# Kernel tuning notes

Hardware: AMD Instinct MI355X
Metric: run time of the kernel (lower is better)

The kernel has to match this reference:

```python
import jax, jax.numpy as jnp
import numpy as np

N, C, R = 100000, 128, 3
NUM_EMB = 3  # ceil((r+1)/2)+1 for r=3
E0, EL = 300000, 80000
SC = 0.05


def setup_inputs() -> dict:
    key = jax.random.key(0)
    ks = jax.random.split(key, 40)
    d = {}
    d["x"] = jax.random.normal(ks[0], (N, C), jnp.float32)
    # loopyN0: row 0 = sorted target node ids (CSR requirement), row 1 = neighbor ids
    t0 = jnp.sort(jax.random.randint(ks[1], (E0,), 0, N))
    s0 = jax.random.randint(ks[2], (E0,), 0, N)
    d["loopyN0"] = jnp.stack([t0, s0]).astype(jnp.int32)
    for L in range(1, R + 1):
        tgt = jnp.sort(jax.random.randint(ks[2 + 2 * L], (EL,), 0, N))
        rest = jax.random.randint(ks[3 + 2 * L], (L + 1, EL), 0, N)
        d[f"loopyN{L}"] = jnp.concatenate([tgt[None], rest]).astype(jnp.int32)
        d[f"loopyA{L}"] = jax.random.randint(ks[10 + L], (L + 2, EL), 0, NUM_EMB).astype(jnp.int32)
    # per-conv params (r=3 unshared CustomGINConv layers), stacked on leading axis
    d["emb"] = jax.random.normal(ks[20], (R, NUM_EMB, C)) * SC
    d["Wt"] = jax.random.normal(ks[21], (R, 2 * C, C)) * SC
    d["bt"] = jax.random.normal(ks[22], (R, C)) * SC
    d["mlp_w0"] = jax.random.normal(ks[23], (R, C, C)) * SC
    d["mlp_b0"] = jax.random.normal(ks[24], (R, C)) * SC
    d["mlp_w1"] = jax.random.normal(ks[25], (R, C, C)) * SC
    d["mlp_b1"] = jax.random.normal(ks[26], (R, C)) * SC
    d["conv_eps"] = jnp.ones((R,), jnp.float32)   # CustomGINConv eps init = ones(1)
    d["r_eps"] = jnp.zeros((R + 1,), jnp.float32)
    d["eps"] = jnp.zeros((), jnp.float32)
    # conv_final: MLP(C, C, num_layers=2, norm=Identity, relu)
    d["fin_w0"] = jax.random.normal(ks[27], (C, C)) * SC
    d["fin_b0"] = jax.random.normal(ks[28], (C,)) * SC
    d["fin_w1"] = jax.random.normal(ks[29], (C, C)) * SC
    d["fin_b1"] = jax.random.normal(ks[30], (C,)) * SC
    return d


def _mlp2(h, w0, b0, w1, b1):
    # MLP with num_layers=2, norm=Identity, relu
    h = h @ w0 + b0
    h = jax.nn.relu(h)
    return h @ w1 + b1


def reference(x, loopyN0, loopyN1, loopyN2, loopyN3, loopyA1, loopyA2, loopyA3,
              emb, Wt, bt, mlp_w0, mlp_b0, mlp_w1, mlp_b1,
              conv_eps, r_eps, eps, fin_w0, fin_b0, fin_w1, fin_b1):
    loopyN = [loopyN0, loopyN1, loopyN2, loopyN3]
    loopyA = [None, loopyA1, loopyA2, loopyA3]
    n_nodes = x.shape[0]
    # L = 0: plain neighbor sum (segment_csr over sorted targets == segment_sum)
    seg = jax.ops.segment_sum(x[loopyN0[1]], loopyN0[0], num_segments=n_nodes)
    rc = (1.0 + r_eps[0]) * seg
    for L in range(1, R + 1):
        nl = loopyN[L]
        cc = x[nl[1:]]                                  # [L+1, E, C] path-node gather
        at = loopyA[L][1:]                              # [L+1, E] atomic types
        i = L - 1
        h = jnp.concatenate([cc, emb[i][at]], axis=-1) @ Wt[i] + bt[i]   # [L+1, E, C]
        # custom_propagate: kernel [1,0,1] along path axis, zero 'same' padding
        hp = jnp.pad(h, ((1, 1), (0, 0), (0, 0)))
        y = hp[:-2] + hp[2:]
        o = _mlp2((1.0 + conv_eps[i]) * cc + y, mlp_w0[i], mlp_b0[i], mlp_w1[i], mlp_b1[i])
        o = o.sum(0)                                    # sum over path positions -> [E, C]
        seg = jax.ops.segment_sum(o, nl[0], num_segments=n_nodes)
        rc = rc + (1.0 + r_eps[L]) * seg
    return _mlp2((1.0 + eps) * x + rc, fin_w0, fin_b0, fin_w1, fin_b1)
```

## Files before the change

### kernel.cpp

```cpp
#include <hip/hip_runtime.h>
#include <stdint.h>

#define CDIM 128
#define NNODES 100000
#define E0EDGES 300000
#define ELEDGES 80000

typedef unsigned short u16;
typedef unsigned int u32;
typedef short bf16x8 __attribute__((ext_vector_type(8)));
typedef float f32x4 __attribute__((ext_vector_type(4)));

__device__ __forceinline__ float bf2f(u32 u){
  union { u32 i; float f; } v; v.i = u << 16; return v.f;
}
__device__ __forceinline__ float bf2f_hi(u32 u){
  union { u32 i; float f; } v; v.i = u & 0xffff0000u; return v.f;
}
__device__ __forceinline__ u16 f2bf(float f){
  u32 u = __builtin_bit_cast(u32, f);
  u32 r = (u + 0x7fffu + ((u >> 16) & 1u)) >> 16;
  return (u16)r;
}
__device__ __forceinline__ u32 pack2(float lo, float hi){
  return ((u32)f2bf(hi) << 16) | (u32)f2bf(lo);
}
__device__ __forceinline__ u32 cvtpk(float lo, float hi){
  u32 r;
  asm("v_cvt_pk_bf16_f32 %0, %1, %2" : "=v"(r) : "v"(lo), "v"(hi));
  return r;
}
template<int CTRL>
__device__ __forceinline__ float dppf(float v){
  int r = __builtin_amdgcn_update_dpp(0, __builtin_bit_cast(int, v), CTRL, 0xF, 0xF, true);
  return __builtin_bit_cast(float, r);
}
#define DPP_SHR1 0x111
#define DPP_SHL1 0x101
#define DPP_XOR1 0xB1
#define DPP_XOR2 0x4E

__device__ __forceinline__ void gll16(const void* g, void* l){
  __builtin_amdgcn_global_load_lds(
      (const __attribute__((address_space(1))) void*)g,
      (__attribute__((address_space(3))) void*)l, 16, 0, 0);
}

__device__ __forceinline__ int swzi(int r, int c){
  return r*CDIM + ((((c>>3) ^ (r&7)))<<3) + (c&7);
}
__device__ __forceinline__ int swz8(int r, int col0){
  int chunk = col0 >> 3;
  return r*CDIM + ((chunk ^ (r & 7)) << 3) + (col0 & 7);
}

__device__ __forceinline__ void gemmT(const u16* W, const u16* A, f32x4 acc[2][4],
                                      int rowbase, int featbase, int lr, int g){
#pragma unroll
  for (int ks = 0; ks < 4; ++ks){
    const int sch = ((ks*4 + g) ^ (lr & 7)) << 3;
    bf16x8 a0 = *(const bf16x8*)&A[(rowbase      + lr)*CDIM + sch];
    bf16x8 a1 = *(const bf16x8*)&A[(rowbase + 16 + lr)*CDIM + sch];
    bf16x8 w0f = *(const bf16x8*)&W[(featbase      + lr)*CDIM + sch];
    bf16x8 w1f = *(const bf16x8*)&W[(featbase + 16 + lr)*CDIM + sch];
    bf16x8 w2f = *(const bf16x8*)&W[(featbase + 32 + lr)*CDIM + sch];
    bf16x8 w3f = *(const bf16x8*)&W[(featbase + 48 + lr)*CDIM + sch];
    acc[0][0] = __builtin_amdgcn_mfma_f32_16x16x32_bf16(w0f, a0, acc[0][0], 0, 0, 0);
    acc[0][1] = __builtin_amdgcn_mfma_f32_16x16x32_bf16(w1f, a0, acc[0][1], 0, 0, 0);
    acc[0][2] = __builtin_amdgcn_mfma_f32_16x16x32_bf16(w2f, a0, acc[0][2], 0, 0, 0);
    acc[0][3] = __builtin_amdgcn_mfma_f32_16x16x32_bf16(w3f, a0, acc[0][3], 0, 0, 0);
    acc[1][0] = __builtin_amdgcn_mfma_f32_16x16x32_bf16(w0f, a1, acc[1][0], 0, 0, 0);
    acc[1][1] = __builtin_amdgcn_mfma_f32_16x16x32_bf16(w1f, a1, acc[1][1], 0, 0, 0);
    acc[1][2] = __builtin_amdgcn_mfma_f32_16x16x32_bf16(w2f, a1, acc[1][2], 0, 0, 0);
    acc[1][3] = __builtin_amdgcn_mfma_f32_16x16x32_bf16(w3f, a1, acc[1][3], 0, 0, 0);
  }
}

__device__ __forceinline__ void gemm64(const u16* A, const u16* B, f32x4* acc, int wave, int lane){
  const int lr = lane & 15, g = lane >> 4;
  const int arow = wave*16 + lr;
#pragma unroll
  for (int ks = 0; ks < 4; ++ks){
    const int ach = ks*4 + g;
    bf16x8 a = *(const bf16x8*)&A[arow*CDIM + ((ach ^ (arow & 7)) << 3)];
#pragma unroll
    for (int ct = 0; ct < 8; ++ct){
      const int brow = ct*16 + lr;
      bf16x8 b = *(const bf16x8*)&B[brow*CDIM + ((ach ^ (brow & 7)) << 3)];
      acc[ct] = __builtin_amdgcn_mfma_f32_16x16x32_bf16(a, b, acc[ct], 0, 0, 0);
    }
  }
}

__device__ __forceinline__ void stage_w(const u16* __restrict__ gsrc, u16* sdst, int tid){
  for (int c = tid; c < CDIM*16; c += 256){
    int r = c >> 4, ch = c & 15;
    *(uint4*)&sdst[(r*16 + (ch ^ (r & 7)))*8] = ((const uint4*)(gsrc + r*CDIM))[ch];
  }
}

__global__ __launch_bounds__(256) void prep_kernel(
    const float* __restrict__ Wt, const float* __restrict__ w0, const float* __restrict__ w1,
    const float* __restrict__ fw0, const float* __restrict__ fw1,
    const float* __restrict__ emb, const float* __restrict__ bt,
    u16* __restrict__ WtS, u16* __restrict__ w0S, u16* __restrict__ w1S,
    u16* __restrict__ fw0T, u16* __restrict__ fw1T, float* __restrict__ eWt)
{
  int tid = blockIdx.x*blockDim.x + threadIdx.x;
  int nt = gridDim.x*blockDim.x;
  for (int idx = tid; idx < 3*CDIM*CDIM; idx += nt){
    int i = idx >> 14, s = idx & 16383;
    int r = s >> 7, ch = ((s >> 3) & 15) ^ (r & 7), k = ch*8 + (s & 7);
    WtS[idx] = f2bf(Wt[(size_t)i*2*CDIM*CDIM + k*CDIM + r]);
    w0S[idx] = f2bf(w0[(size_t)i*CDIM*CDIM + k*CDIM + r]);
    w1S[idx] = f2bf(w1[(size_t)i*CDIM*CDIM + k*CDIM + r]);
  }
  for (int idx = tid; idx < CDIM*CDIM; idx += nt){
    int col = idx/CDIM, k = idx%CDIM;
    fw0T[idx] = f2bf(fw0[k*CDIM + col]);
    fw1T[idx] = f2bf(fw1[k*CDIM + col]);
  }
  for (int idx = tid; idx < 3*3*CDIM; idx += nt){
    int i = idx/(3*CDIM), a = (idx/CDIM)%3, c2 = idx%CDIM;
    float s = bt[i*CDIM + c2];
    for (int k = 0; k < CDIM; ++k)
      s += emb[(i*3 + a)*CDIM + k] * Wt[(size_t)i*2*CDIM*CDIM + (CDIM + k)*CDIM + c2];
    eWt[idx] = s;
  }
}

__global__ __launch_bounds__(256) void aux_kernel(
    const float* __restrict__ x, u16* __restrict__ xb,
    const int* __restrict__ n0, const int* __restrict__ n1,
    const int* __restrict__ n2, const int* __restrict__ n3,
    int* __restrict__ rp0, int* __restrict__ rp1,
    int* __restrict__ rp2, int* __restrict__ rp3,
    u16* __restrict__ zrow)
{
  const int XBQ = NNODES*CDIM/4;
  int gtid = blockIdx.x*256 + threadIdx.x;
  if (gtid < XBQ){
    size_t idx = (size_t)gtid*4;
    float4 v = *(const float4*)(x + idx);
    uint2 o; o.x = cvtpk(v.x, v.y); o.y = cvtpk(v.z, v.w);
    *(uint2*)(xb + idx) = o;
    return;
  }
  int t = gtid - XBQ;
  const int* tgt; int ne; int* rowptr;
  if (t < E0EDGES){ tgt = n0; ne = E0EDGES; rowptr = rp0; }
  else {
    t -= E0EDGES;
    if (t < ELEDGES){ tgt = n1; ne = ELEDGES; rowptr = rp1; }
    else {
      t -= ELEDGES;
      if (t < ELEDGES){ tgt = n2; ne = ELEDGES; rowptr = rp2; }
      else {
        t -= ELEDGES;
        if (t < ELEDGES){ tgt = n3; ne = ELEDGES; rowptr = rp3; }
        else {
          t -= ELEDGES;
          if (t < 64) ((u32*)zrow)[t] = 0u;
          return;
        }
      }
    }
  }
  int e = t;
  int tc = tgt[e];
  int tp = (e == 0) ? -1 : tgt[e-1];
  for (int n = tp + 1; n <= tc; ++n) rowptr[n] = e;
  if (e == ne - 1){
    for (int n = tc + 1; n <= NNODES; ++n) rowptr[n] = ne;
  }
}

template<int L>
__global__ __launch_bounds__(512, 4) void layer_kernel(
    const u16* __restrict__ xb,
    const int* __restrict__ nl,
    const int* __restrict__ ai,
    const u16* __restrict__ WtS, const u16* __restrict__ w0S, const u16* __restrict__ w1S,
    const float* __restrict__ eWt,
    const float* __restrict__ b0g, const float* __restrict__ b1g,
    const float* __restrict__ cepsg,
    const u16* __restrict__ zrow,
    u16* __restrict__ oL)
{
  constexpr int RPE = (L == 1) ? 2 : 4;
  constexpr int TE  = 128 / RPE;
  constexpr int LI  = L - 1;
  __shared__ __align__(16) u16 sW[CDIM*CDIM];
  __shared__ __align__(16) u16 sA[128*CDIM];
  __shared__ __align__(16) float sE[3*136];
  __shared__ __align__(16) float b0s[CDIM];
  __shared__ __align__(16) float b1s[CDIM];
  __shared__ int sAid[128];

  const int tid  = threadIdx.x;
  const int wave = tid >> 6, lane = tid & 63;
  const int lr   = lane & 15, g = lane >> 4;
  const int wr   = wave >> 1, wc = wave & 1;
  const int rowbase  = wr*32;
  const int featbase = wc*64;
  const int e0   = blockIdx.x * TE;
  const int pos  = lr & (RPE - 1);
  const float mu = (pos > 0) ? 1.f : 0.f;
  const float md = (pos < L) ? 1.f : 0.f;
  const float mz = (L == 2 && pos == 3) ? 0.f : 1.f;
  const float ce = 1.0f + cepsg[LI];

  {
    const u16* src = WtS + LI*CDIM*CDIM + wave*4*512 + lane*8;
    u16* dst = sW + wave*4*512;
#pragma unroll
    for (int j = 0; j < 4; ++j) gll16(src + j*512, dst + j*512);
  }
#pragma unroll
  for (int i = 0; i < 4; ++i){
    const int r  = wave*16 + 4*i + (lane >> 4);
    const int p  = r & (RPE - 1);
    const int pc = (p <= L) ? p : 0;
    const int node = nl[(1 + pc)*ELEDGES + e0 + r/RPE];
    const u16* src = (p <= L) ? (xb + (size_t)node*CDIM) : zrow;
    const int cl = lane & 15;
    gll16(src + ((cl ^ (r & 7)) << 3), sA + (wave*16 + 4*i)*CDIM);
  }
  for (int c = tid; c < 3*CDIM; c += 512) sE[(c>>7)*136 + (c&127)] = eWt[LI*3*CDIM + c];
  if (tid < CDIM) b0s[tid] = b0g[LI*CDIM + tid];
  else if (tid < 2*CDIM) b1s[tid-CDIM] = b1g[LI*CDIM + (tid-CDIM)];
  if (tid < 128){
    int p = tid & (RPE - 1);
    sAid[tid] = (p <= L) ? ai[(1 + p)*ELEDGES + e0 + tid/RPE] : 0;
  }
  __syncthreads();

  f32x4 acc[2][4];
#pragma unroll
  for (int a = 0; a < 2; ++a)
#pragma unroll
    for (int b = 0; b < 4; ++b) acc[a][b] = (f32x4){0.f,0.f,0.f,0.f};
  __builtin_amdgcn_s_setprio(1);
  gemmT(sW, sA, acc, rowbase, featbase, lr, g);
  __builtin_amdgcn_s_setprio(0);
  __syncthreads();

  {
    const u16* src = w0S + LI*CDIM*CDIM + wave*4*512 + lane*8;
    u16* dst = sW + wave*4*512;
#pragma unroll
    for (int j = 0; j < 4; ++j) gll16(src + j*512, dst + j*512);
  }
#pragma unroll
  for (int a = 0; a < 2; ++a){
    const int r = rowbase + 16*a + lr;
    const float* eWrow = &sE[sAid[r]*136];
#pragma unroll
    for (int b = 0; b < 4; ++b){
      const int col0 = featbase + 16*b + g*4;
      float4 ew = *(const float4*)&eWrow[col0];
      float h0 = acc[a][b][0] + ew.x;
      float h1 = acc[a][b][1] + ew.y;
      float h2 = acc[a][b][2] + ew.z;
      float h3 = acc[a][b][3] + ew.w;
      float u0 = dppf<DPP_SHR1>(h0), u1 = dppf<DPP_SHR1>(h1),
            u2 = dppf<DPP_SHR1>(h2), u3 = dppf<DPP_SHR1>(h3);
      float d0 = dppf<DPP_SHL1>(h0), d1 = dppf<DPP_SHL1>(h1),
            d2 = dppf<DPP_SHL1>(h2), d3 = dppf<DPP_SHL1>(h3);
      uint2 ccv = *(const uint2*)&sA[swz8(r, col0)];
      float c0 = bf2f(ccv.x & 0xffffu), c1 = bf2f_hi(ccv.x);
      float c2 = bf2f(ccv.y & 0xffffu), c3 = bf2f_hi(ccv.y);
      uint2 zv;
      zv.x = cvtpk(ce*c0 + mu*u0 + md*d0, ce*c1 + mu*u1 + md*d1);
      zv.y = cvtpk(ce*c2 + mu*u2 + md*d2, ce*c3 + mu*u3 + md*d3);
      *(uint2*)&sA[swz8(r, col0)] = zv;
    }
  }
  __syncthreads();

#pragma unroll
  for (int a = 0; a < 2; ++a)
#pragma unroll
    for (int b = 0; b < 4; ++b) acc[a][b] = (f32x4){0.f,0.f,0.f,0.f};
  __builtin_amdgcn_s_setprio(1);
  gemmT(sW, sA, acc, rowbase, featbase, lr, g);
  __builtin_amdgcn_s_setprio(0);
  __syncthreads();

  {
    const u16* src = w1S + LI*CDIM*CDIM + wave*4*512 + lane*8;
    u16* dst = sW + wave*4*512;
#pragma unroll
    for (int j = 0; j < 4; ++j) gll16(src + j*512, dst + j*512);
  }
#pragma unroll
  for (int a = 0; a < 2; ++a){
    const int r = rowbase + 16*a + lr;
#pragma unroll
    for (int b = 0; b < 4; ++b){
      const int col0 = featbase + 16*b + g*4;
      float4 bb = *(const float4*)&b0s[col0];
      float t0 = acc[a][b][0] + bb.x; t0 = t0 > 0.f ? t0 : 0.f;
      float t1 = acc[a][b][1] + bb.y; t1 = t1 > 0.f ? t1 : 0.f;
      float t2 = acc[a][b][2] + bb.z; t2 = t2 > 0.f ? t2 : 0.f;
      float t3 = acc[a][b][3] + bb.w; t3 = t3 > 0.f ? t3 : 0.f;
      uint2 tv; tv.x = cvtpk(t0, t1); tv.y = cvtpk(t2, t3);
      *(uint2*)&sA[swz8(r, col0)] = tv;
    }
  }
  __syncthreads();

#pragma unroll
  for (int a = 0; a < 2; ++a)
#pragma unroll
    for (int b = 0; b < 4; ++b) acc[a][b] = (f32x4){0.f,0.f,0.f,0.f};
  __builtin_amdgcn_s_setprio(1);
  gemmT(sW, sA, acc, rowbase, featbase, lr, g);
  __builtin_amdgcn_s_setprio(0);

  const float nb = (float)(L + 1);
#pragma unroll
  for (int a = 0; a < 2; ++a){
    const int r = rowbase + 16*a + lr;
    const int ed = e0 + r/RPE;
#pragma unroll
    for (int b = 0; b < 4; ++b){
      float v0 = mz*acc[a][b][0], v1 = mz*acc[a][b][1],
            v2 = mz*acc[a][b][2], v3 = mz*acc[a][b][3];
      v0 += dppf<DPP_XOR1>(v0); v1 += dppf<DPP_XOR1>(v1);
      v2 += dppf<DPP_XOR1>(v2); v3 += dppf<DPP_XOR1>(v3);
      if constexpr (RPE == 4){
        v0 += dppf<DPP_XOR2>(v0); v1 += dppf<DPP_XOR2>(v1);
        v2 += dppf<DPP_XOR2>(v2); v3 += dppf<DPP_XOR2>(v3);
      }
      if (pos == 0){
        const int col0 = featbase + 16*b + g*4;
        float4 bb = *(const float4*)&b1s[col0];
        uint2 ov;
        ov.x = cvtpk(v0 + nb*bb.x, v1 + nb*bb.y);
        ov.y = cvtpk(v2 + nb*bb.z, v3 + nb*bb.w);
        *(uint2*)(oL + (size_t)ed*CDIM + col0) = ov;
      }
    }
  }
}

__global__ __launch_bounds__(256) void gather_rc_kernel(
    const float* __restrict__ x, const u16* __restrict__ xbopt,
    const int* __restrict__ s0,
    const int* __restrict__ rp0, const int* __restrict__ rp1,
    const int* __restrict__ rp2, const int* __restrict__ rp3,
    const u16* __restrict__ o1, const u16* __restrict__ o2, const u16* __restrict__ o3,
    const float* __restrict__ repsg, u16* __restrict__ rcb)
{
  const int wave = threadIdx.x >> 6, lane = threadIdx.x & 63;
  const int node = blockIdx.x*4 + wave;
  if (node >= NNODES) return;
  float a0 = 0.f, a1 = 0.f;
  {
    const float sc = 1.f + repsg[0];
    int lo = rp0[node], hi = rp0[node+1];
    if (xbopt){
      for (int e = lo; e < hi; ++e){
        int s = s0[e];
        u32 v = *(const u32*)(xbopt + (size_t)s*CDIM + lane*2);
        a0 += sc*bf2f(v & 0xffffu); a1 += sc*bf2f_hi(v);
      }
    } else {
      for (int e = lo; e < hi; ++e){
        int s = s0[e];
        float2 v = *(const float2*)(x + (size_t)s*CDIM + lane*2);
        a0 += sc*v.x; a1 += sc*v.y;
      }
    }
  }
  const u16* os[3]  = {o1, o2, o3};
  const int* rps[3] = {rp1, rp2, rp3};
#pragma unroll
  for (int li = 0; li < 3; ++li){
    const float sc = 1.f + repsg[1+li];
    int lo = rps[li][node], hi = rps[li][node+1];
    for (int e = lo; e < hi; ++e){
      u32 v = *(const u32*)(os[li] + (size_t)e*CDIM + lane*2);
      a0 += sc*bf2f(v & 0xffffu); a1 += sc*bf2f_hi(v);
    }
  }
  *(u32*)(rcb + (size_t)node*CDIM + lane*2) = pack2(a0, a1);
}

__global__ __launch_bounds__(256) void final_kernel(
    const float* __restrict__ x, const u16* __restrict__ rc,
    const u16* __restrict__ fw0T, const u16* __restrict__ fw1T,
    const float* __restrict__ fb0, const float* __restrict__ fb1,
    const float* __restrict__ epsg, float* __restrict__ outp)
{
  __shared__ __align__(16) u16 sW[CDIM*CDIM];
  __shared__ __align__(16) u16 sA[64*CDIM];
  const int tid  = threadIdx.x;
  const int wave = tid >> 6, lane = tid & 63;
  const int lr   = lane & 15, g = lane >> 4;
  const int r0   = blockIdx.x * 64;
  const float se = 1.0f + epsg[0];

  stage_w(fw0T, sW, tid);
  for (int c = tid; c < 64*16; c += 256){
    int r = c >> 4, ch = c & 15;
    int node = r0 + r;
    uint4 v = make_uint4(0,0,0,0);
    if (node < NNODES){
      const float4* px = (const float4*)(x + (size_t)node*CDIM + ch*8);
      float4 fa = px[0], fb = px[1];
      const u32* pr = (const u32*)(rc + (size_t)node*CDIM + ch*8);
      u32 r0v = pr[0], r1v = pr[1], r2v = pr[2], r3v = pr[3];
      v.x = pack2(se*fa.x + bf2f(r0v & 0xffffu), se*fa.y + bf2f_hi(r0v));
      v.y = pack2(se*fa.z + bf2f(r1v & 0xffffu), se*fa.w + bf2f_hi(r1v));
      v.z = pack2(se*fb.x + bf2f(r2v & 0xffffu), se*fb.y + bf2f_hi(r2v));
      v.w = pack2(se*fb.z + bf2f(r3v & 0xffffu), se*fb.w + bf2f_hi(r3v));
    }
    *(uint4*)&sA[(r*16 + (ch ^ (r & 7)))*8] = v;
  }
  __syncthreads();

  f32x4 acc[8];
#pragma unroll
  for (int ct = 0; ct < 8; ++ct) acc[ct] = (f32x4){0.f,0.f,0.f,0.f};
  gemm64(sA, sW, acc, wave, lane);
  __syncthreads();
#pragma unroll
  for (int ct = 0; ct < 8; ++ct){
    const int col = ct*16 + lr;
    const float bb = fb0[col];
#pragma unroll
    for (int q = 0; q < 4; ++q){
      const int r = wave*16 + g*4 + q;
      float t = acc[ct][q] + bb;
      t = t > 0.f ? t : 0.f;
      sA[swzi(r, col)] = f2bf(t);
    }
  }
  stage_w(fw1T, sW, tid);
  __syncthreads();
#pragma unroll
  for (int ct = 0; ct < 8; ++ct) acc[ct] = (f32x4){0.f,0.f,0.f,0.f};
  gemm64(sA, sW, acc, wave, lane);
#pragma unroll
  for (int ct = 0; ct < 8; ++ct){
    const int col = ct*16 + lr;
    const float bb = fb1[col];
#pragma unroll
    for (int q = 0; q < 4; ++q){
      const int r = wave*16 + g*4 + q;
      int node = r0 + r;
      if (node < NNODES) outp[(size_t)node*CDIM + col] = acc[ct][q] + bb;
    }
  }
}

extern "C" void kernel_launch(void* const* d_in, const int* in_sizes, int n_in,
                              void* d_out, int out_size, void* d_ws, size_t ws_size,
                              hipStream_t stream)
{
  const float* x   = (const float*)d_in[0];
  const int* n0    = (const int*)d_in[1];
  const int* n1    = (const int*)d_in[2];
  const int* a1    = (const int*)d_in[3];
  const int* n2    = (const int*)d_in[4];
  const int* a2    = (const int*)d_in[5];
  const int* n3    = (const int*)d_in[6];
  const int* a3    = (const int*)d_in[7];
  const float* emb = (const float*)d_in[8];
  const float* Wt  = (const float*)d_in[9];
  const float* bt  = (const float*)d_in[10];
  const float* w0  = (const float*)d_in[11];
  const float* b0  = (const float*)d_in[12];
  const float* w1  = (const float*)d_in[13];
  const float* b1  = (const float*)d_in[14];
  const float* ceps= (const float*)d_in[15];
  const float* reps= (const float*)d_in[16];
  const float* eps = (const float*)d_in[17];
  const float* fw0 = (const float*)d_in[18];
  const float* fb0 = (const float*)d_in[19];
  const float* fw1 = (const float*)d_in[20];
  const float* fb1 = (const float*)d_in[21];
  float* outp = (float*)d_out;

  char* w = (char*)d_ws;
  size_t off = 0;
  auto alloc = [&](size_t bytes) -> char* {
    char* p = w + off;
    off += (bytes + 255) & ~((size_t)255);
    return p;
  };
  u16* o1   = (u16*)alloc((size_t)ELEDGES*CDIM*2);
  u16* o2   = (u16*)alloc((size_t)ELEDGES*CDIM*2);
  u16* o3   = (u16*)alloc((size_t)ELEDGES*CDIM*2);
  u16* rcb  = (u16*)alloc((size_t)NNODES*CDIM*2);
  int* rp0  = (int*)alloc((size_t)(NNODES+1)*4);
  int* rp1  = (int*)alloc((size_t)(NNODES+1)*4);
  int* rp2  = (int*)alloc((size_t)(NNODES+1)*4);
  int* rp3  = (int*)alloc((size_t)(NNODES+1)*4);
  u16* WtS  = (u16*)alloc((size_t)3*CDIM*CDIM*2);
  u16* w0S  = (u16*)alloc((size_t)3*CDIM*CDIM*2);
  u16* w1S  = (u16*)alloc((size_t)3*CDIM*CDIM*2);
  u16* fw0T = (u16*)alloc((size_t)CDIM*CDIM*2);
  u16* fw1T = (u16*)alloc((size_t)CDIM*CDIM*2);
  float* eWt = (float*)alloc((size_t)3*3*CDIM*4);
  u16* zrow = (u16*)alloc((size_t)CDIM*2);
  const size_t xbbytes = (size_t)NNODES*CDIM*2;
  u16* xb; const u16* xbopt;
  if (off + xbbytes <= ws_size){ xb = (u16*)alloc(xbbytes); xbopt = xb; }
  else { xb = rcb; xbopt = nullptr; }
  (void)in_sizes; (void)n_in; (void)out_size;

  prep_kernel<<<192, 256, 0, stream>>>(Wt, w0, w1, fw0, fw1, emb, bt,
                                       WtS, w0S, w1S, fw0T, fw1T, eWt);
  {
    const int XBQ = NNODES*CDIM/4;
    int total = XBQ + E0EDGES + 3*ELEDGES + 64;
    aux_kernel<<<(total + 255)/256, 256, 0, stream>>>(x, xb, n0, n1, n2, n3,
                                                      rp0, rp1, rp2, rp3, zrow);
  }

  layer_kernel<1><<<ELEDGES/64, 512, 0, stream>>>(xb, n1, a1, WtS, w0S, w1S, eWt, b0, b1, ceps, zrow, o1);
  layer_kernel<2><<<ELEDGES/32, 512, 0, stream>>>(xb, n2, a2, WtS, w0S, w1S, eWt, b0, b1, ceps, zrow, o2);
  layer_kernel<3><<<ELEDGES/32, 512, 0, stream>>>(xb, n3, a3, WtS, w0S, w1S, eWt, b0, b1, ceps, zrow, o3);

  gather_rc_kernel<<<(NNODES+3)/4, 256, 0, stream>>>(x, xbopt, n0 + E0EDGES, rp0, rp1, rp2, rp3,
                                                     o1, o2, o3, reps, rcb);
  final_kernel<<<(NNODES+63)/64, 256, 0, stream>>>(x, rcb, fw0T, fw1T, fb0, fb1, eps, outp);
}
```

Measured before the change: 393.0 us.

## Merge prep/aux and three layer kernels into single launches; vectorize gather

Folds the weight-prep kernel into the aux kernel and combines the three per-layer launches into one kernel that picks the layer from the block index. This cuts launch overhead and lets work from different layers overlap on the device. The gather kernel now splits each node's edges across four lane groups, loading 16 bytes per lane and combining the partial sums with shuffles. The final kernel reads the bf16 copy of x instead of fp32 x, which halves that read but adds rounding error to the x term.

```diff
diff --git a/kernel.cpp b/kernel.cpp
--- a/kernel.cpp
+++ b/kernel.cpp
@@ -99,103 +99,97 @@
   }
 }
 
-__global__ __launch_bounds__(256) void prep_kernel(
-    const float* __restrict__ Wt, const float* __restrict__ w0, const float* __restrict__ w1,
-    const float* __restrict__ fw0, const float* __restrict__ fw1,
-    const float* __restrict__ emb, const float* __restrict__ bt,
-    u16* __restrict__ WtS, u16* __restrict__ w0S, u16* __restrict__ w1S,
-    u16* __restrict__ fw0T, u16* __restrict__ fw1T, float* __restrict__ eWt)
-{
-  int tid = blockIdx.x*blockDim.x + threadIdx.x;
-  int nt = gridDim.x*blockDim.x;
-  for (int idx = tid; idx < 3*CDIM*CDIM; idx += nt){
-    int i = idx >> 14, s = idx & 16383;
-    int r = s >> 7, ch = ((s >> 3) & 15) ^ (r & 7), k = ch*8 + (s & 7);
-    WtS[idx] = f2bf(Wt[(size_t)i*2*CDIM*CDIM + k*CDIM + r]);
-    w0S[idx] = f2bf(w0[(size_t)i*CDIM*CDIM + k*CDIM + r]);
-    w1S[idx] = f2bf(w1[(size_t)i*CDIM*CDIM + k*CDIM + r]);
-  }
-  for (int idx = tid; idx < CDIM*CDIM; idx += nt){
-    int col = idx/CDIM, k = idx%CDIM;
-    fw0T[idx] = f2bf(fw0[k*CDIM + col]);
-    fw1T[idx] = f2bf(fw1[k*CDIM + col]);
-  }
-  for (int idx = tid; idx < 3*3*CDIM; idx += nt){
-    int i = idx/(3*CDIM), a = (idx/CDIM)%3, c2 = idx%CDIM;
-    float s = bt[i*CDIM + c2];
-    for (int k = 0; k < CDIM; ++k)
-      s += emb[(i*3 + a)*CDIM + k] * Wt[(size_t)i*2*CDIM*CDIM + (CDIM + k)*CDIM + c2];
-    eWt[idx] = s;
-  }
-}
-
-__global__ __launch_bounds__(256) void aux_kernel(
+__global__ __launch_bounds__(256) void prep_aux_kernel(
     const float* __restrict__ x, u16* __restrict__ xb,
     const int* __restrict__ n0, const int* __restrict__ n1,
     const int* __restrict__ n2, const int* __restrict__ n3,
     int* __restrict__ rp0, int* __restrict__ rp1,
     int* __restrict__ rp2, int* __restrict__ rp3,
+    const float* __restrict__ Wt, const float* __restrict__ w0, const float* __restrict__ w1,
+    const float* __restrict__ fw0, const float* __restrict__ fw1,
+    const float* __restrict__ emb, const float* __restrict__ bt,
+    u16* __restrict__ WtS, u16* __restrict__ w0S, u16* __restrict__ w1S,
+    u16* __restrict__ fw0T, u16* __restrict__ fw1T, float* __restrict__ eWt,
     u16* __restrict__ zrow)
 {
-  const int XBQ = NNODES*CDIM/4;
-  int gtid = blockIdx.x*256 + threadIdx.x;
-  if (gtid < XBQ){
-    size_t idx = (size_t)gtid*4;
+  const int XBQ  = NNODES*CDIM/4;
+  const int NCSR = E0EDGES + 3*ELEDGES;
+  const int NW   = 3*CDIM*CDIM;
+  const int NF   = CDIM*CDIM;
+  const int NE   = 3*3*CDIM;
+  int t = blockIdx.x*256 + threadIdx.x;
+  if (t < XBQ){
+    size_t idx = (size_t)t*4;
     float4 v = *(const float4*)(x + idx);
     uint2 o; o.x = cvtpk(v.x, v.y); o.y = cvtpk(v.z, v.w);
     *(uint2*)(xb + idx) = o;
     return;
   }
-  int t = gtid - XBQ;
-  const int* tgt; int ne; int* rowptr;
-  if (t < E0EDGES){ tgt = n0; ne = E0EDGES; rowptr = rp0; }
-  else {
-    t -= E0EDGES;
-    if (t < ELEDGES){ tgt = n1; ne = ELEDGES; rowptr = rp1; }
-    else {
-      t -= ELEDGES;
-      if (t < ELEDGES){ tgt = n2; ne = ELEDGES; rowptr = rp2; }
-      else {
-        t -= ELEDGES;
-        if (t < ELEDGES){ tgt = n3; ne = ELEDGES; rowptr = rp3; }
-        else {
-          t -= ELEDGES;
-          if (t < 64) ((u32*)zrow)[t] = 0u;
-          return;
-        }
-      }
-    }
-  }
-  int e = t;
-  int tc = tgt[e];
-  int tp = (e == 0) ? -1 : tgt[e-1];
-  for (int n = tp + 1; n <= tc; ++n) rowptr[n] = e;
-  if (e == ne - 1){
-    for (int n = tc + 1; n <= NNODES; ++n) rowptr[n] = ne;
-  }
+  t -= XBQ;
+  if (t < NCSR){
+    const int* tgt; int ne; int* rowptr;
+    if (t < E0EDGES){ tgt = n0; ne = E0EDGES; rowptr = rp0; }
+    else { t -= E0EDGES;
+      if (t < ELEDGES){ tgt = n1; ne = ELEDGES; rowptr = rp1; }
+      else { t -= ELEDGES;
+        if (t < ELEDGES){ tgt = n2; ne = ELEDGES; rowptr = rp2; }
+        else { t -= ELEDGES; tgt = n3; ne = ELEDGES; rowptr = rp3; }
+      }
+    }
+    int e = t;
+    int tc = tgt[e];
+    int tp = (e == 0) ? -1 : tgt[e-1];
+    for (int n = tp + 1; n <= tc; ++n) rowptr[n] = e;
+    if (e == ne - 1){
+      for (int n = tc + 1; n <= NNODES; ++n) rowptr[n] = ne;
+    }
+    return;
+  }
+  t -= NCSR;
+  if (t < NW){
+    int i = t >> 14, s = t & 16383;
+    int r = s >> 7, ch = ((s >> 3) & 15) ^ (r & 7), k = ch*8 + (s & 7);
+    WtS[t] = f2bf(Wt[(size_t)i*2*CDIM*CDIM + k*CDIM + r]);
+    w0S[t] = f2bf(w0[(size_t)i*CDIM*CDIM + k*CDIM + r]);
+    w1S[t] = f2bf(w1[(size_t)i*CDIM*CDIM + k*CDIM + r]);
+    return;
+  }
+  t -= NW;
+  if (t < NF){
+    int col = t/CDIM, k = t%CDIM;
+    fw0T[t] = f2bf(fw0[k*CDIM + col]);
+    fw1T[t] = f2bf(fw1[k*CDIM + col]);
+    return;
+  }
+  t -= NF;
+  if (t < NE){
+    int i = t/(3*CDIM), a = (t/CDIM)%3, c2 = t%CDIM;
+    float s = bt[i*CDIM + c2];
+    for (int k = 0; k < CDIM; ++k)
+      s += emb[(i*3 + a)*CDIM + k] * Wt[(size_t)i*2*CDIM*CDIM + (CDIM + k)*CDIM + c2];
+    eWt[t] = s;
+    return;
+  }
+  t -= NE;
+  if (t < 64) ((u32*)zrow)[t] = 0u;
 }
 
 template<int L>
-__global__ __launch_bounds__(512, 4) void layer_kernel(
+__device__ __forceinline__ void layer_body(
+    int bidx,
     const u16* __restrict__ xb,
-    const int* __restrict__ nl,
-    const int* __restrict__ ai,
+    const int* __restrict__ nl, const int* __restrict__ ai,
     const u16* __restrict__ WtS, const u16* __restrict__ w0S, const u16* __restrict__ w1S,
     const float* __restrict__ eWt,
     const float* __restrict__ b0g, const float* __restrict__ b1g,
     const float* __restrict__ cepsg,
     const u16* __restrict__ zrow,
-    u16* __restrict__ oL)
+    u16* __restrict__ oL,
+    u16* sW, u16* sA, float* sE, float* b0s, float* b1s, int* sAid)
 {
   constexpr int RPE = (L == 1) ? 2 : 4;
   constexpr int TE  = 128 / RPE;
   constexpr int LI  = L - 1;
-  __shared__ __align__(16) u16 sW[CDIM*CDIM];
-  __shared__ __align__(16) u16 sA[128*CDIM];
-  __shared__ __align__(16) float sE[3*136];
-  __shared__ __align__(16) float b0s[CDIM];
-  __shared__ __align__(16) float b1s[CDIM];
-  __shared__ int sAid[128];
 
   const int tid  = threadIdx.x;
   const int wave = tid >> 6, lane = tid & 63;
@@ -203,7 +197,7 @@
   const int wr   = wave >> 1, wc = wave & 1;
   const int rowbase  = wr*32;
   const int featbase = wc*64;
-  const int e0   = blockIdx.x * TE;
+  const int e0   = bidx * TE;
   const int pos  = lr & (RPE - 1);
   const float mu = (pos > 0) ? 1.f : 0.f;
   const float md = (pos < L) ? 1.f : 0.f;
@@ -345,6 +339,38 @@
   }
 }
 
+__global__ __launch_bounds__(512, 4) void layers_kernel(
+    const u16* __restrict__ xb,
+    const int* __restrict__ n1, const int* __restrict__ a1,
+    const int* __restrict__ n2, const int* __restrict__ a2,
+    const int* __restrict__ n3, const int* __restrict__ a3,
+    const u16* __restrict__ WtS, const u16* __restrict__ w0S, const u16* __restrict__ w1S,
+    const float* __restrict__ eWt,
+    const float* __restrict__ b0g, const float* __restrict__ b1g,
+    const float* __restrict__ cepsg,
+    const u16* __restrict__ zrow,
+    u16* __restrict__ o1, u16* __restrict__ o2, u16* __restrict__ o3)
+{
+  __shared__ __align__(16) u16 sW[CDIM*CDIM];
+  __shared__ __align__(16) u16 sA[128*CDIM];
+  __shared__ __align__(16) float sE[3*136];
+  __shared__ __align__(16) float b0s[CDIM];
+  __shared__ __align__(16) float b1s[CDIM];
+  __shared__ int sAid[128];
+  constexpr int NB1 = ELEDGES/64;
+  constexpr int NB2 = ELEDGES/32;
+  const int b = blockIdx.x;
+  if (b < NB1)
+    layer_body<1>(b, xb, n1, a1, WtS, w0S, w1S, eWt, b0g, b1g, cepsg, zrow, o1,
+                  sW, sA, sE, b0s, b1s, sAid);
+  else if (b < NB1 + NB2)
+    layer_body<2>(b - NB1, xb, n2, a2, WtS, w0S, w1S, eWt, b0g, b1g, cepsg, zrow, o2,
+                  sW, sA, sE, b0s, b1s, sAid);
+  else
+    layer_body<3>(b - NB1 - NB2, xb, n3, a3, WtS, w0S, w1S, eWt, b0g, b1g, cepsg, zrow, o3,
+                  sW, sA, sE, b0s, b1s, sAid);
+}
+
 __global__ __launch_bounds__(256) void gather_rc_kernel(
     const float* __restrict__ x, const u16* __restrict__ xbopt,
     const int* __restrict__ s0,
@@ -356,40 +382,79 @@
   const int wave = threadIdx.x >> 6, lane = threadIdx.x & 63;
   const int node = blockIdx.x*4 + wave;
   if (node >= NNODES) return;
-  float a0 = 0.f, a1 = 0.f;
-  {
-    const float sc = 1.f + repsg[0];
-    int lo = rp0[node], hi = rp0[node+1];
-    if (xbopt){
-      for (int e = lo; e < hi; ++e){
+  if (xbopt){
+    const int lr = lane & 15, gg = lane >> 4;
+    float a0=0.f,a1=0.f,a2=0.f,a3=0.f,a4=0.f,a5=0.f,a6=0.f,a7=0.f;
+    {
+      const float sc = 1.f + repsg[0];
+      const int lo = rp0[node], hi = rp0[node+1];
+      for (int e = lo + gg; e < hi; e += 4){
         int s = s0[e];
-        u32 v = *(const u32*)(xbopt + (size_t)s*CDIM + lane*2);
-        a0 += sc*bf2f(v & 0xffffu); a1 += sc*bf2f_hi(v);
-      }
-    } else {
+        uint4 v = *(const uint4*)(xbopt + (size_t)s*CDIM + lr*8);
+        a0 = fmaf(sc, bf2f(v.x & 0xffffu), a0); a1 = fmaf(sc, bf2f_hi(v.x), a1);
+        a2 = fmaf(sc, bf2f(v.y & 0xffffu), a2); a3 = fmaf(sc, bf2f_hi(v.y), a3);
+        a4 = fmaf(sc, bf2f(v.z & 0xffffu), a4); a5 = fmaf(sc, bf2f_hi(v.z), a5);
+        a6 = fmaf(sc, bf2f(v.w & 0xffffu), a6); a7 = fmaf(sc, bf2f_hi(v.w), a7);
+      }
+    }
+    const u16* os[3]  = {o1, o2, o3};
+    const int* rps[3] = {rp1, rp2, rp3};
+#pragma unroll
+    for (int li = 0; li < 3; ++li){
+      const float sc = 1.f + repsg[1+li];
+      const int lo = rps[li][node], hi = rps[li][node+1];
+      const u16* ob = os[li];
+      for (int e = lo + gg; e < hi; e += 4){
+        uint4 v = *(const uint4*)(ob + (size_t)e*CDIM + lr*8);
+        a0 = fmaf(sc, bf2f(v.x & 0xffffu), a0); a1 = fmaf(sc, bf2f_hi(v.x), a1);
+        a2 = fmaf(sc, bf2f(v.y & 0xffffu), a2); a3 = fmaf(sc, bf2f_hi(v.y), a3);
+        a4 = fmaf(sc, bf2f(v.z & 0xffffu), a4); a5 = fmaf(sc, bf2f_hi(v.z), a5);
+        a6 = fmaf(sc, bf2f(v.w & 0xffffu), a6); a7 = fmaf(sc, bf2f_hi(v.w), a7);
+      }
+    }
+    a0 += __shfl_xor(a0, 16, 64); a1 += __shfl_xor(a1, 16, 64);
+    a2 += __shfl_xor(a2, 16, 64); a3 += __shfl_xor(a3, 16, 64);
+    a4 += __shfl_xor(a4, 16, 64); a5 += __shfl_xor(a5, 16, 64);
+    a6 += __shfl_xor(a6, 16, 64); a7 += __shfl_xor(a7, 16, 64);
+    a0 += __shfl_xor(a0, 32, 64); a1 += __shfl_xor(a1, 32, 64);
+    a2 += __shfl_xor(a2, 32, 64); a3 += __shfl_xor(a3, 32, 64);
+    a4 += __shfl_xor(a4, 32, 64); a5 += __shfl_xor(a5, 32, 64);
+    a6 += __shfl_xor(a6, 32, 64); a7 += __shfl_xor(a7, 32, 64);
+    if (gg == 0){
+      uint4 ov;
+      ov.x = cvtpk(a0, a1); ov.y = cvtpk(a2, a3);
+      ov.z = cvtpk(a4, a5); ov.w = cvtpk(a6, a7);
+      *(uint4*)(rcb + (size_t)node*CDIM + lr*8) = ov;
+    }
+  } else {
+    float a0 = 0.f, a1 = 0.f;
+    {
+      const float sc = 1.f + repsg[0];
+      int lo = rp0[node], hi = rp0[node+1];
       for (int e = lo; e < hi; ++e){
         int s = s0[e];
         float2 v = *(const float2*)(x + (size_t)s*CDIM + lane*2);
         a0 += sc*v.x; a1 += sc*v.y;
       }
     }
-  }
-  const u16* os[3]  = {o1, o2, o3};
-  const int* rps[3] = {rp1, rp2, rp3};
-#pragma unroll
-  for (int li = 0; li < 3; ++li){
-    const float sc = 1.f + repsg[1+li];
-    int lo = rps[li][node], hi = rps[li][node+1];
-    for (int e = lo; e < hi; ++e){
-      u32 v = *(const u32*)(os[li] + (size_t)e*CDIM + lane*2);
-      a0 += sc*bf2f(v & 0xffffu); a1 += sc*bf2f_hi(v);
-    }
-  }
-  *(u32*)(rcb + (size_t)node*CDIM + lane*2) = pack2(a0, a1);
+    const u16* os[3]  = {o1, o2, o3};
+    const int* rps[3] = {rp1, rp2, rp3};
+#pragma unroll
+    for (int li = 0; li < 3; ++li){
+      const float sc = 1.f + repsg[1+li];
+      int lo = rps[li][node], hi = rps[li][node+1];
+      for (int e = lo; e < hi; ++e){
+        u32 v = *(const u32*)(os[li] + (size_t)e*CDIM + lane*2);
+        a0 += sc*bf2f(v & 0xffffu); a1 += sc*bf2f_hi(v);
+      }
+    }
+    *(u32*)(rcb + (size_t)node*CDIM + lane*2) = pack2(a0, a1);
+  }
 }
 
 __global__ __launch_bounds__(256) void final_kernel(
-    const float* __restrict__ x, const u16* __restrict__ rc,
+    const float* __restrict__ x, const u16* __restrict__ xbopt,
+    const u16* __restrict__ rc,
     const u16* __restrict__ fw0T, const u16* __restrict__ fw1T,
     const float* __restrict__ fb0, const float* __restrict__ fb1,
     const float* __restrict__ epsg, float* __restrict__ outp)
@@ -408,14 +473,22 @@
     int node = r0 + r;
     uint4 v = make_uint4(0,0,0,0);
     if (node < NNODES){
-      const float4* px = (const float4*)(x + (size_t)node*CDIM + ch*8);
-      float4 fa = px[0], fb = px[1];
       const u32* pr = (const u32*)(rc + (size_t)node*CDIM + ch*8);
       u32 r0v = pr[0], r1v = pr[1], r2v = pr[2], r3v = pr[3];
-      v.x = pack2(se*fa.x + bf2f(r0v & 0xffffu), se*fa.y + bf2f_hi(r0v));
-      v.y = pack2(se*fa.z + bf2f(r1v & 0xffffu), se*fa.w + bf2f_hi(r1v));
-      v.z = pack2(se*fb.x + bf2f(r2v & 0xffffu), se*fb.y + bf2f_hi(r2v));
-      v.w = pack2(se*fb.z + bf2f(r3v & 0xffffu), se*fb.w + bf2f_hi(r3v));
+      if (xbopt){
+        uint4 xv = *(const uint4*)(xbopt + (size_t)node*CDIM + ch*8);
+        v.x = cvtpk(se*bf2f(xv.x & 0xffffu) + bf2f(r0v & 0xffffu), se*bf2f_hi(xv.x) + bf2f_hi(r0v));
+        v.y = cvtpk(se*bf2f(xv.y & 0xffffu) + bf2f(r1v & 0xffffu), se*bf2f_hi(xv.y) + bf2f_hi(r1v));
+        v.z = cvtpk(se*bf2f(xv.z & 0xffffu) + bf2f(r2v & 0xffffu), se*bf2f_hi(xv.z) + bf2f_hi(r2v));
+        v.w = cvtpk(se*bf2f(xv.w & 0xffffu) + bf2f(r3v & 0xffffu), se*bf2f_hi(xv.w) + bf2f_hi(r3v));
+      } else {
+        const float4* px = (const float4*)(x + (size_t)node*CDIM + ch*8);
+        float4 fa = px[0], fb = px[1];
+        v.x = pack2(se*fa.x + bf2f(r0v & 0xffffu), se*fa.y + bf2f_hi(r0v));
+        v.y = pack2(se*fa.z + bf2f(r1v & 0xffffu), se*fa.w + bf2f_hi(r1v));
+        v.z = pack2(se*fb.x + bf2f(r2v & 0xffffu), se*fb.y + bf2f_hi(r2v));
+        v.w = pack2(se*fb.z + bf2f(r3v & 0xffffu), se*fb.w + bf2f_hi(r3v));
+      }
     }
     *(uint4*)&sA[(r*16 + (ch ^ (r & 7)))*8] = v;
   }
@@ -512,20 +585,19 @@
   else { xb = rcb; xbopt = nullptr; }
   (void)in_sizes; (void)n_in; (void)out_size;
 
-  prep_kernel<<<192, 256, 0, stream>>>(Wt, w0, w1, fw0, fw1, emb, bt,
-                                       WtS, w0S, w1S, fw0T, fw1T, eWt);
   {
     const int XBQ = NNODES*CDIM/4;
-    int total = XBQ + E0EDGES + 3*ELEDGES + 64;
-    aux_kernel<<<(total + 255)/256, 256, 0, stream>>>(x, xb, n0, n1, n2, n3,
-                                                      rp0, rp1, rp2, rp3, zrow);
-  }
-
-  layer_kernel<1><<<ELEDGES/64, 512, 0, stream>>>(xb, n1, a1, WtS, w0S, w1S, eWt, b0, b1, ceps, zrow, o1);
-  layer_kernel<2><<<ELEDGES/32, 512, 0, stream>>>(xb, n2, a2, WtS, w0S, w1S, eWt, b0, b1, ceps, zrow, o2);
-  layer_kernel<3><<<ELEDGES/32, 512, 0, stream>>>(xb, n3, a3, WtS, w0S, w1S, eWt, b0, b1, ceps, zrow, o3);
+    int total = XBQ + (E0EDGES + 3*ELEDGES) + 3*CDIM*CDIM + CDIM*CDIM + 3*3*CDIM + 64;
+    prep_aux_kernel<<<(total + 255)/256, 256, 0, stream>>>(
+        x, xb, n0, n1, n2, n3, rp0, rp1, rp2, rp3,
+        Wt, w0, w1, fw0, fw1, emb, bt,
+        WtS, w0S, w1S, fw0T, fw1T, eWt, zrow);
+  }
+
+  layers_kernel<<<ELEDGES/64 + 2*(ELEDGES/32), 512, 0, stream>>>(
+      xb, n1, a1, n2, a2, n3, a3, WtS, w0S, w1S, eWt, b0, b1, ceps, zrow, o1, o2, o3);
 
   gather_rc_kernel<<<(NNODES+3)/4, 256, 0, stream>>>(x, xbopt, n0 + E0EDGES, rp0, rp1, rp2, rp3,
                                                      o1, o2, o3, reps, rcb);
-  final_kernel<<<(NNODES+63)/64, 256, 0, stream>>>(x, rcb, fw0T, fw1T, fb0, fb1, eps, outp);
-}
+  final_kernel<<<(NNODES+63)/64, 256, 0, stream>>>(x, xbopt, rcb, fw0T, fw1T, fb0, fb1, eps, outp);
+}
```

Result: faster. 362.2 us (-7.8%).
